# Kernel optimization log

Measured on AMD Instinct MI355X. Metric: run time of the kernel, lower is better.

The kernel has to match this reference:

```python
import jax, jax.numpy as jnp
import numpy as np

N_NODES = 100000
TYPE_COUNTS = [40000, 40000, 20000]
RAW_DIMS = [512, 256, 128]
D = 64          # node_feature_dim
H = 8           # num_attention_heads
M = 2           # num_metapaths
E = 500000      # edges per metapath
SEM = 128       # semantic_attention_dim
NUM_CLS = 8
T = 40000       # num target nodes
SLOPE = 0.01    # leaky relu slope


def setup_inputs() -> dict:
    key = jax.random.key(0)
    ks = jax.random.split(key, 16)
    inp = {}
    inp['target_nodes'] = jax.random.randint(ks[0], (T,), 0, N_NODES)
    inp['metapath_0'] = jax.random.randint(ks[1], (E, 2), 0, N_NODES)
    inp['metapath_1'] = jax.random.randint(ks[2], (E, 2), 0, N_NODES)
    # contiguous blocks per node type (type t occupies a contiguous index range)
    inp['node_type_mapping'] = jnp.concatenate(
        [jnp.full((c,), t, dtype=jnp.int32) for t, c in enumerate(TYPE_COUNTS)])
    for t, (c, r) in enumerate(zip(TYPE_COUNTS, RAW_DIMS)):
        inp[f'node_feat_{t}'] = jax.random.normal(ks[3 + t], (c, r), dtype=jnp.float32)
        xav = float(np.sqrt(2.0) * np.sqrt(2.0 / (D + r)))
        inp[f'W{t}'] = jax.random.normal(ks[6 + t], (D, r), dtype=jnp.float32) * xav
        inp[f'b{t}'] = jnp.zeros((D,), dtype=jnp.float32)
    inp['node_attention'] = jax.random.normal(ks[9], (M, H, 2 * D), dtype=jnp.float32) * 0.05
    inp['Wsem'] = jax.random.normal(ks[10], (SEM, H * D), dtype=jnp.float32) * 0.05
    inp['bsem'] = jnp.zeros((SEM,), dtype=jnp.float32)
    inp['a_sem'] = jax.random.normal(ks[11], (SEM,), dtype=jnp.float32) * 0.05
    inp['Wcls'] = jax.random.normal(ks[12], (NUM_CLS, H * D), dtype=jnp.float32) * 0.05
    inp['bcls'] = jnp.zeros((NUM_CLS,), dtype=jnp.float32)
    return inp


def _metapath_agg(node_features, mp, attn_vec, target_nodes, n_nodes):
    # mp: [E, 2] (col 0 = neighbor/src, col -1 = current/dst); attn_vec: [H, 2D]
    src = mp[:, 0]
    dst = mp[:, -1]
    h_src = node_features[src]                        # [E, D] gather
    h_dst = node_features[dst]                        # [E, D] gather
    e = jnp.concatenate([h_dst, h_src], axis=-1)      # [E, 2D]
    score = e @ attn_vec.T                            # [E, H]
    score = jnp.where(score > 0, score, SLOPE * score)  # LeakyReLU
    # edge softmax over incoming edges of each destination node (per head)
    m = jax.ops.segment_max(score, dst, num_segments=n_nodes)
    ex = jnp.exp(score - m[dst])
    den = jax.ops.segment_sum(ex, dst, num_segments=n_nodes)
    attn = ex / den[dst]                              # [E, H]
    weighted = h_src[:, None, :] * attn[:, :, None]   # [E, H, D]
    agg = jax.ops.segment_sum(weighted, dst, num_segments=n_nodes)  # [N, H, D]
    return agg[target_nodes]                          # [T, H, D]


def reference(target_nodes, metapath_0, metapath_1, node_type_mapping,
              node_feat_0, node_feat_1, node_feat_2,
              W0, b0, W1, b1, W2, b2,
              node_attention, Wsem, bsem, a_sem, Wcls, bcls):
    n_nodes = node_type_mapping.shape[0]
    # node types are contiguous index blocks, so per-type projection + concat
    # reproduces the original scatter-by-type exactly (dropout rate is 0)
    node_features = jnp.concatenate([
        node_feat_0 @ W0.T + b0,
        node_feat_1 @ W1.T + b1,
        node_feat_2 @ W2.T + b2,
    ], axis=0)                                        # [N, D]
    h_list = [
        _metapath_agg(node_features, metapath_0, node_attention[0], target_nodes, n_nodes),
        _metapath_agg(node_features, metapath_1, node_attention[1], target_nodes, n_nodes),
    ]
    h = jnp.stack(h_list).reshape(M, -1, H * D)       # [M, T, H*D]
    s = jnp.tanh(jnp.einsum('mtd,sd->mts', h, Wsem) + bsem)  # [M, T, SEM]
    scores = jnp.mean(s @ a_sem, axis=1)              # [M] semantic attention
    beta = jax.nn.softmax(scores)                     # [M]
    embeddings = jnp.einsum('m,mtd->td', beta, h)     # [T, H*D]
    cls_logits = embeddings @ Wcls.T + bcls           # [T, NUM_CLS]
    return cls_logits, embeddings
```

## Files before the change

kernel.cpp:

```cpp
#include <hip/hip_runtime.h>
#include <hip/hip_bf16.h>

#define N_NODES 100000
#define EDGES   500000
#define T_TGT   40000
#define NH      8
#define NSEM    128
#define NCLS    8
#define SLOPE   0.01f
#define NCHUNK  25

typedef __attribute__((ext_vector_type(8))) __bf16 bf16x8;
typedef __attribute__((ext_vector_type(4))) float f32x4;

__global__ __launch_bounds__(256) void proj_gemm(const float* __restrict__ A,
        const float* __restrict__ W, const float* __restrict__ bias,
        float* __restrict__ out, int M, int K) {
    __shared__ float As[32][68];
    __shared__ float Ws[32][68];
    int tid = threadIdx.x;
    int r0 = blockIdx.x * 64;
    int ty = tid >> 4;
    int tx = tid & 15;
    float acc[4][4] = {};
    for (int kk = 0; kk < K; kk += 32) {
        #pragma unroll
        for (int i = 0; i < 2; i++) {
            int lin = tid + i * 256;
            int row = lin >> 3;
            int c4 = (lin & 7) * 4;
            float4 v = make_float4(0.f, 0.f, 0.f, 0.f);
            if (r0 + row < M)
                v = *(const float4*)(A + (size_t)(r0 + row) * K + kk + c4);
            As[c4 + 0][row] = v.x; As[c4 + 1][row] = v.y;
            As[c4 + 2][row] = v.z; As[c4 + 3][row] = v.w;
            float4 w = *(const float4*)(W + (size_t)row * K + kk + c4);
            Ws[c4 + 0][row] = w.x; Ws[c4 + 1][row] = w.y;
            Ws[c4 + 2][row] = w.z; Ws[c4 + 3][row] = w.w;
        }
        __syncthreads();
        #pragma unroll
        for (int k = 0; k < 32; k++) {
            float4 a4 = *(const float4*)&As[k][ty * 4];
            float4 b4 = *(const float4*)&Ws[k][tx * 4];
            float a[4] = {a4.x, a4.y, a4.z, a4.w};
            float b[4] = {b4.x, b4.y, b4.z, b4.w};
            #pragma unroll
            for (int i = 0; i < 4; i++)
                #pragma unroll
                for (int j = 0; j < 4; j++)
                    acc[i][j] = fmaf(a[i], b[j], acc[i][j]);
        }
        __syncthreads();
    }
    float4 b4 = *(const float4*)(bias + tx * 4);
    #pragma unroll
    for (int i = 0; i < 4; i++) {
        int r = r0 + ty * 4 + i;
        if (r < M) {
            float4 o = make_float4(acc[i][0] + b4.x, acc[i][1] + b4.y,
                                   acc[i][2] + b4.z, acc[i][3] + b4.w);
            *(float4*)(out + (size_t)r * 64 + tx * 4) = o;
        }
    }
}

__global__ __launch_bounds__(256) void attn_proj(const float* __restrict__ nf,
        const float* __restrict__ na, float* __restrict__ proj) {
    __shared__ float ft[64][65];
    __shared__ float at[32][65];
    int tid = threadIdx.x;
    int n0 = blockIdx.x * 64;
    #pragma unroll
    for (int i = 0; i < 8; i++) {
        int lin = tid + i * 256;
        int j = lin >> 6, d = lin & 63;
        int m = j >> 4, side = (j >> 3) & 1, h = j & 7;
        at[j][d] = na[m * 1024 + h * 128 + side * 64 + d];
    }
    #pragma unroll
    for (int i = 0; i < 4; i++) {
        int lin = tid + i * 256;
        int row = lin >> 4;
        int c4 = (lin & 15) * 4;
        int gn = n0 + row;
        float4 v = make_float4(0.f, 0.f, 0.f, 0.f);
        if (gn < N_NODES) v = *(const float4*)(nf + (size_t)gn * 64 + c4);
        ft[row][c4 + 0] = v.x; ft[row][c4 + 1] = v.y;
        ft[row][c4 + 2] = v.z; ft[row][c4 + 3] = v.w;
    }
    __syncthreads();
    int node = tid >> 2;
    int jg = tid & 3;
    float acc[8] = {};
    for (int d = 0; d < 64; d++) {
        float f = ft[node][d];
        #pragma unroll
        for (int jj = 0; jj < 8; jj++)
            acc[jj] = fmaf(f, at[jg * 8 + jj][d], acc[jj]);
    }
    int gn = n0 + node;
    if (gn < N_NODES) {
        float4 o0 = make_float4(acc[0], acc[1], acc[2], acc[3]);
        float4 o1 = make_float4(acc[4], acc[5], acc[6], acc[7]);
        *(float4*)(proj + (size_t)gn * 32 + jg * 8) = o0;
        *(float4*)(proj + (size_t)gn * 32 + jg * 8 + 4) = o1;
    }
}

__global__ void hist_targets(const int* __restrict__ tgt, int* __restrict__ tcnt) {
    int i = blockIdx.x * 256 + threadIdx.x;
    if (i < T_TGT) atomicAdd(&tcnt[tgt[i]], 1);
}

__global__ void hist_edges(const int* __restrict__ mp, const int* __restrict__ tcnt,
                           int* __restrict__ ecnt) {
    int e = blockIdx.x * 256 + threadIdx.x;
    if (e < EDGES) {
        int dst = mp[2 * e + 1];
        if (tcnt[dst] > 0) atomicAdd(&ecnt[dst], 1);
    }
}

__global__ __launch_bounds__(1024) void scan_partial(const int* __restrict__ counts,
        int* __restrict__ partials) {
    int a = blockIdx.y, bx = blockIdx.x;
    const int* in = counts + (size_t)a * N_NODES;
    int base = bx * 4096 + threadIdx.x * 4;
    int s = 0;
    #pragma unroll
    for (int i = 0; i < 4; i++) {
        int idx = base + i;
        if (idx < N_NODES) s += in[idx];
    }
    #pragma unroll
    for (int off = 32; off; off >>= 1) s += __shfl_xor(s, off);
    __shared__ int red[16];
    int lane = threadIdx.x & 63, w = threadIdx.x >> 6;
    if (lane == 0) red[w] = s;
    __syncthreads();
    if (threadIdx.x < 16) {
        int x = red[threadIdx.x];
        #pragma unroll
        for (int off = 8; off; off >>= 1) x += __shfl_xor(x, off);
        if (threadIdx.x == 0) partials[a * 32 + bx] = x;
    }
}

__global__ void scan_partials(const int* __restrict__ partials,
        int* __restrict__ choff, int* __restrict__ offs) {
    int w = threadIdx.x >> 6, lane = threadIdx.x & 63;
    if (w < 3 && lane < 32) {
        int v = (lane < NCHUNK) ? partials[w * 32 + lane] : 0;
        int x = v;
        #pragma unroll
        for (int off = 1; off < 32; off <<= 1) {
            int y = __shfl_up(x, off);
            if (lane >= off) x += y;
        }
        if (lane < NCHUNK) choff[w * 32 + lane] = x - v;
        if (lane == NCHUNK - 1) offs[(size_t)w * (N_NODES + 1) + N_NODES] = x;
    }
}

__global__ __launch_bounds__(1024) void scan_final(const int* __restrict__ counts,
        const int* __restrict__ choff, int* __restrict__ offs, int* __restrict__ curs) {
    int a = blockIdx.y, bx = blockIdx.x;
    const int* in = counts + (size_t)a * N_NODES;
    int* out = offs + (size_t)a * (N_NODES + 1);
    int* cur = curs + (size_t)a * N_NODES;
    int tid = threadIdx.x, lane = tid & 63, w = tid >> 6;
    int base = bx * 4096 + tid * 4;
    int v[4], sum4 = 0;
    #pragma unroll
    for (int i = 0; i < 4; i++) {
        int idx = base + i;
        v[i] = (idx < N_NODES) ? in[idx] : 0;
        sum4 += v[i];
    }
    int x = sum4;
    #pragma unroll
    for (int off = 1; off < 64; off <<= 1) {
        int y = __shfl_up(x, off);
        if (lane >= off) x += y;
    }
    __shared__ int wred[16], wexc[16];
    if (lane == 63) wred[w] = x;
    __syncthreads();
    if (tid < 16) {
        int s = wred[tid], xs = s;
        #pragma unroll
        for (int off = 1; off < 16; off <<= 1) {
            int y = __shfl_up(xs, off);
            if (tid >= off) xs += y;
        }
        wexc[tid] = xs - s;
    }
    __syncthreads();
    int off0 = choff[a * 32 + bx] + wexc[w] + (x - sum4);
    int run = 0;
    #pragma unroll
    for (int i = 0; i < 4; i++) {
        int idx = base + i;
        if (idx < N_NODES) { out[idx] = off0 + run; cur[idx] = off0 + run; }
        run += v[i];
    }
}

__global__ void scatter_targets(const int* __restrict__ tgt, int* __restrict__ tcur,
                                int* __restrict__ tlist) {
    int i = blockIdx.x * 256 + threadIdx.x;
    if (i < T_TGT) {
        int n = tgt[i];
        int p = atomicAdd(&tcur[n], 1);
        tlist[p] = i;
    }
}

__global__ __launch_bounds__(256) void scatter_score(const int* __restrict__ mp,
        const int* __restrict__ tcnt, int* __restrict__ ecur,
        int* __restrict__ elist, __bf16* __restrict__ exs,
        const float* __restrict__ proj, int m) {
    int e = blockIdx.x * 256 + threadIdx.x;
    if (e >= EDGES) return;
    int src = mp[2 * e], dst = mp[2 * e + 1];
    if (tcnt[dst] <= 0) return;
    int p = atomicAdd(&ecur[dst], 1);
    elist[p] = src;
    const float* adp = proj + (size_t)dst * 32 + m * 16;
    const float* asp = proj + (size_t)src * 32 + m * 16 + 8;
    float4 ad0 = *(const float4*)(adp), ad1 = *(const float4*)(adp + 4);
    float4 as0 = *(const float4*)(asp), as1 = *(const float4*)(asp + 4);
    float ads[8] = {ad0.x, ad0.y, ad0.z, ad0.w, ad1.x, ad1.y, ad1.z, ad1.w};
    float ass[8] = {as0.x, as0.y, as0.z, as0.w, as1.x, as1.y, as1.z, as1.w};
    bf16x8 exv;
    #pragma unroll
    for (int h = 0; h < 8; h++) {
        float sc = ads[h] + ass[h];
        sc = sc > 0.f ? sc : SLOPE * sc;
        exv[h] = (__bf16)__expf(sc);
    }
    *(bf16x8*)(exs + (size_t)p * 8) = exv;
}

__global__ void build_ulist(const int* __restrict__ tcnt, int* __restrict__ ulist,
                            int* __restrict__ ucount) {
    int n = blockIdx.x * 256 + threadIdx.x;
    if (n < N_NODES && tcnt[n] > 0) {
        int u = atomicAdd(ucount, 1);
        ulist[u] = n;
    }
}

__global__ void cvt_bf16(const float* __restrict__ in, __bf16* __restrict__ out, int n) {
    int i = blockIdx.x * 256 + threadIdx.x;
    if (i < n) out[i] = (__bf16)in[i];
}

__global__ __launch_bounds__(256) void agg_kernel(
        const int* __restrict__ ulist, const int* __restrict__ ctrl_i,
        const int* __restrict__ offs,
        const int* __restrict__ esrc,
        const __bf16* __restrict__ exs,
        const float* __restrict__ nf,
        const int* __restrict__ tlist,
        __bf16* hb0, __bf16* hb1) {
    int m = blockIdx.y;
    int wslot = blockIdx.x * 4 + (threadIdx.x >> 6);
    int lane = threadIdx.x & 63;
    int ucount = ctrl_i[0];
    if (wslot >= ucount) return;
    int node = __builtin_amdgcn_readfirstlane(ulist[wslot]);
    const int* eo = offs + (size_t)m * (N_NODES + 1);
    int e0 = eo[node], e1 = eo[node + 1];
    const int* srcs = esrc + (size_t)m * EDGES;
    const __bf16* exm = exs + (size_t)m * EDGES * 8;
    float acc[8] = {};
    float dacc[8] = {};
    for (int e = e0; e < e1; e++) {
        int s = srcs[e];
        bf16x8 pb = *(const bf16x8*)(exm + (size_t)e * 8);
        float v = nf[(size_t)s * 64 + lane];
        #pragma unroll
        for (int h = 0; h < 8; h++) {
            float pw = (float)pb[h];
            dacc[h] += pw;
            acc[h] = fmaf(pw, v, acc[h]);
        }
    }
    #pragma unroll
    for (int h = 0; h < 8; h++)
        acc[h] *= (dacc[h] > 0.f) ? 1.0f / dacc[h] : 0.f;
    const int* to = offs + (size_t)2 * (N_NODES + 1);
    int t0 = to[node], t1 = to[node + 1];
    __bf16* hb = (m == 0) ? hb0 : hb1;
    for (int ti = t0; ti < t1; ti++) {
        int t = tlist[ti];
        __bf16* dst = hb + (size_t)t * 512;
        #pragma unroll
        for (int h = 0; h < 8; h++) dst[h * 64 + lane] = (__bf16)acc[h];
    }
}

__global__ __launch_bounds__(256) void sem_mfma(
        const __bf16* __restrict__ hb,
        const __bf16* __restrict__ Wb,
        const float* __restrict__ bsem, const float* __restrict__ a_sem,
        float* __restrict__ scores) {
    int m = blockIdx.y;
    const __bf16* A = hb + (size_t)m * T_TGT * 512 + (size_t)blockIdx.x * 64 * 512;
    int wave = threadIdx.x >> 6, lane = threadIdx.x & 63;
    int n0 = wave * 32;
    int mrow = lane & 15;
    int koff0 = (lane >> 4) * 8;
    f32x4 acc[4][2] = {};
    for (int k0 = 0; k0 < 512; k0 += 32) {
        int koff = k0 + koff0;
        bf16x8 a[4], b[2];
        #pragma unroll
        for (int r = 0; r < 4; r++)
            a[r] = *(const bf16x8*)(A + (size_t)(r * 16 + mrow) * 512 + koff);
        #pragma unroll
        for (int c = 0; c < 2; c++)
            b[c] = *(const bf16x8*)(Wb + (size_t)(n0 + c * 16 + mrow) * 512 + koff);
        #pragma unroll
        for (int r = 0; r < 4; r++)
            #pragma unroll
            for (int c = 0; c < 2; c++)
                acc[r][c] = __builtin_amdgcn_mfma_f32_16x16x32_bf16(a[r], b[c], acc[r][c], 0, 0, 0);
    }
    float tot = 0.f;
    #pragma unroll
    for (int c = 0; c < 2; c++) {
        int col = n0 + c * 16 + (lane & 15);
        float bs = bsem[col], as = a_sem[col];
        #pragma unroll
        for (int r = 0; r < 4; r++)
            #pragma unroll
            for (int j = 0; j < 4; j++) {
                float x = acc[r][c][j] + bs;
                float th = 1.f - 2.f / (__expf(2.f * x) + 1.f);
                tot += th * as;
            }
    }
    __shared__ float red[256];
    red[threadIdx.x] = tot;
    __syncthreads();
    for (int s = 128; s; s >>= 1) {
        if (threadIdx.x < s) red[threadIdx.x] += red[threadIdx.x + s];
        __syncthreads();
    }
    if (threadIdx.x == 0) atomicAdd(&scores[m], red[0]);
}

__global__ void beta_kernel(const float* __restrict__ scores, float* __restrict__ beta) {
    if (threadIdx.x == 0) {
        float s0 = scores[0] / (float)T_TGT;
        float s1 = scores[1] / (float)T_TGT;
        float mx = fmaxf(s0, s1);
        float e0 = __expf(s0 - mx), e1 = __expf(s1 - mx);
        float inv = 1.f / (e0 + e1);
        beta[0] = e0 * inv;
        beta[1] = e1 * inv;
    }
}

__global__ __launch_bounds__(256) void emb_cls(
        const __bf16* __restrict__ hb0, const __bf16* __restrict__ hb1,
        const float* __restrict__ beta, const float* __restrict__ Wcls,
        const float* __restrict__ bcls, float* out_cls, float* out_emb) {
    __shared__ float Wl[8 * 512];
    int tid = threadIdx.x;
    #pragma unroll
    for (int i = 0; i < 16; i++) Wl[tid + i * 256] = Wcls[tid + i * 256];
    __syncthreads();
    int t = blockIdx.x * 4 + (tid >> 6);
    int lane = tid & 63;
    float b0 = beta[0], b1 = beta[1];
    bf16x8 v0 = *(const bf16x8*)(hb0 + (size_t)t * 512 + lane * 8);
    bf16x8 v1 = *(const bf16x8*)(hb1 + (size_t)t * 512 + lane * 8);
    float e[8];
    #pragma unroll
    for (int j = 0; j < 8; j++) e[j] = b0 * (float)v0[j] + b1 * (float)v1[j];
    float* ep = out_emb + (size_t)t * 512 + lane * 8;
    *(float4*)(ep + 0) = make_float4(e[0], e[1], e[2], e[3]);
    *(float4*)(ep + 4) = make_float4(e[4], e[5], e[6], e[7]);
    float pc[8];
    #pragma unroll
    for (int c = 0; c < 8; c++) {
        float4 w0 = *(const float4*)(Wl + c * 512 + lane * 8);
        float4 w1 = *(const float4*)(Wl + c * 512 + lane * 8 + 4);
        pc[c] = e[0] * w0.x + e[1] * w0.y + e[2] * w0.z + e[3] * w0.w
              + e[4] * w1.x + e[5] * w1.y + e[6] * w1.z + e[7] * w1.w;
    }
    #pragma unroll
    for (int off = 32; off; off >>= 1)
        #pragma unroll
        for (int c = 0; c < 8; c++) pc[c] += __shfl_xor(pc[c], off);
    if (lane == 0) {
        #pragma unroll
        for (int c = 0; c < 8; c++) out_cls[(size_t)t * 8 + c] = pc[c] + bcls[c];
    }
}

extern "C" void kernel_launch(void* const* d_in, const int* in_sizes, int n_in,
                              void* d_out, int out_size, void* d_ws, size_t ws_size,
                              hipStream_t stream) {
    const int* target = (const int*)d_in[0];
    const int* mp0 = (const int*)d_in[1];
    const int* mp1 = (const int*)d_in[2];
    const float* feat0 = (const float*)d_in[4];
    const float* W0 = (const float*)d_in[5];
    const float* b0 = (const float*)d_in[6];
    const float* feat1 = (const float*)d_in[7];
    const float* W1 = (const float*)d_in[8];
    const float* b1 = (const float*)d_in[9];
    const float* feat2 = (const float*)d_in[10];
    const float* W2 = (const float*)d_in[11];
    const float* b2 = (const float*)d_in[12];
    const float* natt = (const float*)d_in[13];
    const float* Wsem = (const float*)d_in[14];
    const float* bsem = (const float*)d_in[15];
    const float* asem = (const float*)d_in[16];
    const float* Wcls = (const float*)d_in[17];
    const float* bcls = (const float*)d_in[18];

    char* ws = (char*)d_ws;
    size_t off = 0;
    auto alloc = [&](size_t bytes) -> void* {
        void* p = ws + off;
        off += (bytes + 31) & ~(size_t)31;
        return p;
    };
    float* nf    = (float*)alloc((size_t)N_NODES * 64 * 4);
    float* proj  = (float*)alloc((size_t)N_NODES * 32 * 4);
    int* counts3 = (int*)alloc((size_t)3 * N_NODES * 4);
    int* offs3   = (int*)alloc((size_t)3 * (N_NODES + 1) * 4);
    int* curs3   = (int*)alloc((size_t)3 * N_NODES * 4);
    int* tlist   = (int*)alloc((size_t)T_TGT * 4);
    int* ulist   = (int*)alloc((size_t)N_NODES * 4);
    int* esrc    = (int*)alloc((size_t)2 * EDGES * 4);
    __bf16* exs  = (__bf16*)alloc((size_t)2 * EDGES * 8 * 2);
    int* partials = (int*)alloc((size_t)3 * 32 * 4);
    int* choff    = (int*)alloc((size_t)3 * 32 * 4);
    int* ctrl    = (int*)alloc(64);
    __bf16* Wsem_b = (__bf16*)alloc((size_t)NSEM * 512 * 2);
    __bf16* hb   = (__bf16*)alloc((size_t)2 * T_TGT * 512 * 2);
    if (off > ws_size) return;

    float* out_cls = (float*)d_out;
    float* out_emb = out_cls + (size_t)T_TGT * NCLS;
    __bf16* hb0 = hb;
    __bf16* hb1 = hb + (size_t)T_TGT * 512;
    float* ctrl_f = (float*)ctrl;
    float* scores = ctrl_f + 1;
    float* beta = ctrl_f + 3;

    hipMemsetAsync(counts3, 0, (size_t)3 * N_NODES * 4, stream);
    hipMemsetAsync(ctrl, 0, 64, stream);

    proj_gemm<<<dim3(625), 256, 0, stream>>>(feat0, W0, b0, nf, 40000, 512);
    proj_gemm<<<dim3(625), 256, 0, stream>>>(feat1, W1, b1, nf + (size_t)40000 * 64, 40000, 256);
    proj_gemm<<<dim3(313), 256, 0, stream>>>(feat2, W2, b2, nf + (size_t)80000 * 64, 20000, 128);
    attn_proj<<<dim3(1563), 256, 0, stream>>>(nf, natt, proj);
    cvt_bf16<<<dim3(256), 256, 0, stream>>>(Wsem, Wsem_b, NSEM * 512);

    hist_targets<<<dim3(157), 256, 0, stream>>>(target, counts3 + 2 * N_NODES);
    hist_edges<<<dim3(1954), 256, 0, stream>>>(mp0, counts3 + 2 * N_NODES, counts3);
    hist_edges<<<dim3(1954), 256, 0, stream>>>(mp1, counts3 + 2 * N_NODES, counts3 + N_NODES);
    scan_partial<<<dim3(NCHUNK, 3), 1024, 0, stream>>>(counts3, partials);
    scan_partials<<<dim3(1), 192, 0, stream>>>(partials, choff, offs3);
    scan_final<<<dim3(NCHUNK, 3), 1024, 0, stream>>>(counts3, choff, offs3, curs3);
    scatter_targets<<<dim3(157), 256, 0, stream>>>(target, curs3 + 2 * N_NODES, tlist);
    scatter_score<<<dim3(1954), 256, 0, stream>>>(mp0, counts3 + 2 * N_NODES, curs3,
                                                  esrc, exs, proj, 0);
    scatter_score<<<dim3(1954), 256, 0, stream>>>(mp1, counts3 + 2 * N_NODES, curs3 + N_NODES,
                                                  esrc + EDGES, exs + (size_t)EDGES * 8, proj, 1);
    build_ulist<<<dim3(391), 256, 0, stream>>>(counts3 + 2 * N_NODES, ulist, ctrl);

    agg_kernel<<<dim3(10000, 2), 256, 0, stream>>>(ulist, ctrl, offs3, esrc, exs,
                                                   nf, tlist, hb0, hb1);
    sem_mfma<<<dim3(625, 2), 256, 0, stream>>>(hb, Wsem_b, bsem, asem, scores);
    beta_kernel<<<dim3(1), 64, 0, stream>>>(scores, beta);
    emb_cls<<<dim3(10000), 256, 0, stream>>>(hb0, hb1, beta, Wcls, bcls, out_cls, out_emb);
}
```

Baseline: 527.4 us.

## Store aggregated target features in MFMA-friendly tiled layout for semantic GEMM

The per-target bf16 aggregation buffer moves from row-major [T,512] to a tiled layout of 16-row blocks, with 8-element k-chunks interleaved across rows. This lets sem_mfma load each A fragment as one contiguous 16-byte-per-lane access. sem_mfma now computes 32 rows per block over twice as many blocks, and emb_cls is rewritten to read the tiled layout, handling 16 targets per block with a shared-memory reduction for the classifier. Writes in agg_kernel become more scattered, and emb_cls's output writes are less coalesced.

```diff
diff --git a/kernel.cpp b/kernel.cpp
--- a/kernel.cpp
+++ b/kernel.cpp
@@ -12,6 +12,7 @@
 
 typedef __attribute__((ext_vector_type(8))) __bf16 bf16x8;
 typedef __attribute__((ext_vector_type(4))) float f32x4;
+
 
 __global__ __launch_bounds__(256) void proj_gemm(const float* __restrict__ A,
         const float* __restrict__ W, const float* __restrict__ bias,
@@ -294,11 +295,12 @@
     const int* to = offs + (size_t)2 * (N_NODES + 1);
     int t0 = to[node], t1 = to[node + 1];
     __bf16* hb = (m == 0) ? hb0 : hb1;
+    int widx = (lane >> 3) * 128 + (lane & 7);
     for (int ti = t0; ti < t1; ti++) {
         int t = tlist[ti];
-        __bf16* dst = hb + (size_t)t * 512;
-        #pragma unroll
-        for (int h = 0; h < 8; h++) dst[h * 64 + lane] = (__bf16)acc[h];
+        __bf16* dst = hb + (size_t)(t >> 4) * 8192 + (t & 15) * 8 + widx;
+        #pragma unroll
+        for (int h = 0; h < 8; h++) dst[h * 1024] = (__bf16)acc[h];
     }
 }
 
@@ -308,26 +310,27 @@
         const float* __restrict__ bsem, const float* __restrict__ a_sem,
         float* __restrict__ scores) {
     int m = blockIdx.y;
-    const __bf16* A = hb + (size_t)m * T_TGT * 512 + (size_t)blockIdx.x * 64 * 512;
+    const __bf16* A = hb + (size_t)m * T_TGT * 512;
     int wave = threadIdx.x >> 6, lane = threadIdx.x & 63;
     int n0 = wave * 32;
     int mrow = lane & 15;
     int koff0 = (lane >> 4) * 8;
-    f32x4 acc[4][2] = {};
+    size_t tb0 = (size_t)(blockIdx.x * 2) * 8192 + lane * 8;
+    f32x4 acc[2][2] = {};
+    #pragma unroll
     for (int k0 = 0; k0 < 512; k0 += 32) {
-        int koff = k0 + koff0;
-        bf16x8 a[4], b[2];
-        #pragma unroll
-        for (int r = 0; r < 4; r++)
-            a[r] = *(const bf16x8*)(A + (size_t)(r * 16 + mrow) * 512 + koff);
+        bf16x8 a[2], b[2];
+        #pragma unroll
+        for (int rt = 0; rt < 2; rt++)
+            a[rt] = *(const bf16x8*)(A + tb0 + rt * 8192 + k0 * 16);
         #pragma unroll
         for (int c = 0; c < 2; c++)
-            b[c] = *(const bf16x8*)(Wb + (size_t)(n0 + c * 16 + mrow) * 512 + koff);
-        #pragma unroll
-        for (int r = 0; r < 4; r++)
+            b[c] = *(const bf16x8*)(Wb + (size_t)(n0 + c * 16 + mrow) * 512 + k0 + koff0);
+        #pragma unroll
+        for (int rt = 0; rt < 2; rt++)
             #pragma unroll
             for (int c = 0; c < 2; c++)
-                acc[r][c] = __builtin_amdgcn_mfma_f32_16x16x32_bf16(a[r], b[c], acc[r][c], 0, 0, 0);
+                acc[rt][c] = __builtin_amdgcn_mfma_f32_16x16x32_bf16(a[rt], b[c], acc[rt][c], 0, 0, 0);
     }
     float tot = 0.f;
     #pragma unroll
@@ -335,10 +338,10 @@
         int col = n0 + c * 16 + (lane & 15);
         float bs = bsem[col], as = a_sem[col];
         #pragma unroll
-        for (int r = 0; r < 4; r++)
+        for (int rt = 0; rt < 2; rt++)
             #pragma unroll
             for (int j = 0; j < 4; j++) {
-                float x = acc[r][c][j] + bs;
+                float x = acc[rt][c][j] + bs;
                 float th = 1.f - 2.f / (__expf(2.f * x) + 1.f);
                 tot += th * as;
             }
@@ -370,36 +373,44 @@
         const float* __restrict__ beta, const float* __restrict__ Wcls,
         const float* __restrict__ bcls, float* out_cls, float* out_emb) {
     __shared__ float Wl[8 * 512];
+    __shared__ float pls[256 * 9];
     int tid = threadIdx.x;
     #pragma unroll
     for (int i = 0; i < 16; i++) Wl[tid + i * 256] = Wcls[tid + i * 256];
     __syncthreads();
-    int t = blockIdx.x * 4 + (tid >> 6);
-    int lane = tid & 63;
+    int t0 = blockIdx.x * 16;
+    size_t tb = (size_t)blockIdx.x * 8192;
     float b0 = beta[0], b1 = beta[1];
-    bf16x8 v0 = *(const bf16x8*)(hb0 + (size_t)t * 512 + lane * 8);
-    bf16x8 v1 = *(const bf16x8*)(hb1 + (size_t)t * 512 + lane * 8);
-    float e[8];
-    #pragma unroll
-    for (int j = 0; j < 8; j++) e[j] = b0 * (float)v0[j] + b1 * (float)v1[j];
-    float* ep = out_emb + (size_t)t * 512 + lane * 8;
-    *(float4*)(ep + 0) = make_float4(e[0], e[1], e[2], e[3]);
-    *(float4*)(ep + 4) = make_float4(e[4], e[5], e[6], e[7]);
-    float pc[8];
-    #pragma unroll
-    for (int c = 0; c < 8; c++) {
-        float4 w0 = *(const float4*)(Wl + c * 512 + lane * 8);
-        float4 w1 = *(const float4*)(Wl + c * 512 + lane * 8 + 4);
-        pc[c] = e[0] * w0.x + e[1] * w0.y + e[2] * w0.z + e[3] * w0.w
-              + e[4] * w1.x + e[5] * w1.y + e[6] * w1.z + e[7] * w1.w;
-    }
-    #pragma unroll
-    for (int off = 32; off; off >>= 1)
-        #pragma unroll
-        for (int c = 0; c < 8; c++) pc[c] += __shfl_xor(pc[c], off);
-    if (lane == 0) {
-        #pragma unroll
-        for (int c = 0; c < 8; c++) out_cls[(size_t)t * 8 + c] = pc[c] + bcls[c];
+    int r = tid & 15;
+    float pc[8] = {};
+    #pragma unroll
+    for (int j = 0; j < 4; j++) {
+        int i2 = tid + j * 256;
+        int kb = i2 >> 4;
+        bf16x8 v0 = *(const bf16x8*)(hb0 + tb + (size_t)i2 * 8);
+        bf16x8 v1 = *(const bf16x8*)(hb1 + tb + (size_t)i2 * 8);
+        float e[8];
+        #pragma unroll
+        for (int q = 0; q < 8; q++) e[q] = b0 * (float)v0[q] + b1 * (float)v1[q];
+        float* ep = out_emb + (size_t)(t0 + r) * 512 + kb * 8;
+        *(float4*)(ep + 0) = make_float4(e[0], e[1], e[2], e[3]);
+        *(float4*)(ep + 4) = make_float4(e[4], e[5], e[6], e[7]);
+        #pragma unroll
+        for (int c = 0; c < 8; c++) {
+            const float* w = Wl + c * 512 + kb * 8;
+            #pragma unroll
+            for (int q = 0; q < 8; q++) pc[c] = fmaf(e[q], w[q], pc[c]);
+        }
+    }
+    #pragma unroll
+    for (int c = 0; c < 8; c++) pls[tid * 9 + c] = pc[c];
+    __syncthreads();
+    if (tid < 128) {
+        int rr = tid & 15, c = tid >> 4;
+        float s = 0.f;
+        #pragma unroll
+        for (int k = 0; k < 16; k++) s += pls[(rr + 16 * k) * 9 + c];
+        out_cls[(size_t)(t0 + rr) * 8 + c] = s + bcls[c];
     }
 }
 
@@ -480,7 +491,7 @@
 
     agg_kernel<<<dim3(10000, 2), 256, 0, stream>>>(ulist, ctrl, offs3, esrc, exs,
                                                    nf, tlist, hb0, hb1);
-    sem_mfma<<<dim3(625, 2), 256, 0, stream>>>(hb, Wsem_b, bsem, asem, scores);
+    sem_mfma<<<dim3(1250, 2), 256, 0, stream>>>(hb, Wsem_b, bsem, asem, scores);
     beta_kernel<<<dim3(1), 64, 0, stream>>>(scores, beta);
-    emb_cls<<<dim3(10000), 256, 0, stream>>>(hb0, hb1, beta, Wcls, bcls, out_cls, out_emb);
-}
+    emb_cls<<<dim3(2500), 256, 0, stream>>>(hb0, hb1, beta, Wcls, bcls, out_cls, out_emb);
+}
```

After: 636.2 us. 20.6% more time.
